# Optimization experiments

Hardware: AMD Instinct MI355X
Metric: run time of the kernel (lower is better)

The kernel has to match this reference:

```python
import jax, jax.numpy as jnp
import numpy as np

N = 100000   # nodes
E = 600000   # edges
G = 512      # graphs in batch
EPS = 1e-5   # LayerNorm eps
IN_DIM = 60 + 2 + 12  # dyn feats*frames + dims + st embedding
H = 128


def setup_inputs() -> dict:
    key = jax.random.key(0)
    ks = jax.random.split(key, 32)
    inp = {
        "x": jax.random.normal(ks[0], (N, 60), jnp.float32),
        "xdims": jax.random.uniform(ks[1], (N, 2), jnp.float32),
        "xsttype": jax.random.randint(ks[2], (N,), 0, 256, jnp.int32),
        "edge_index": jax.random.randint(ks[3], (2, E), 0, N, jnp.int32),
        "batch": jnp.sort(jax.random.randint(ks[4], (N,), 0, G, jnp.int32)),
        "emb": jax.random.normal(ks[5], (256, 12), jnp.float32),
    }
    def lin(k, i, o):
        s = 1.0 / np.sqrt(i)
        return jax.random.uniform(k, (i, o), jnp.float32, -s, s)
    dims = [IN_DIM, H, H]
    for l in range(2):
        i, o = dims[l], dims[l + 1]
        inp[f"Wl{l}"] = lin(ks[6 + 4 * l], i, o)   # lin_l: applied to aggregated neighbors
        inp[f"bl{l}"] = jnp.zeros((o,), jnp.float32)
        inp[f"Wr{l}"] = lin(ks[7 + 4 * l], i, o)   # lin_r: applied to root (no bias, PyG SAGEConv)
        inp[f"g{l}"] = jnp.ones((o,), jnp.float32)   # LayerNorm gamma
        inp[f"bn{l}"] = jnp.zeros((o,), jnp.float32)  # LayerNorm beta
    ld = [2 * H, 50, 50, 10]
    for l in range(3):
        inp[f"Wf{l}"] = lin(ks[20 + l], ld[l], ld[l + 1])
        inp[f"bf{l}"] = jnp.zeros((ld[l + 1],), jnp.float32)
    return inp


def _layer_norm(h, g, b):
    mu = jnp.mean(h, axis=-1, keepdims=True)
    var = jnp.mean(jnp.square(h - mu), axis=-1, keepdims=True)
    return (h - mu) * jax.lax.rsqrt(var + EPS) * g + b


def reference(x, xdims, xsttype, edge_index, batch, emb,
              Wl0, bl0, Wr0, g0, bn0,
              Wl1, bl1, Wr1, g1, bn1,
              Wf0, bf0, Wf1, bf1, Wf2, bf2):
    # node feature assembly: [N, 60+2+12]
    h = jnp.concatenate([x, xdims, emb[xsttype]], axis=1)

    src, dst = edge_index[0], edge_index[1]
    deg = jax.ops.segment_sum(jnp.ones((E,), h.dtype), dst, num_segments=N)
    inv_deg = (1.0 / jnp.maximum(deg, 1.0))[:, None]

    for Wl, bl, Wr, g, bn in ((Wl0, bl0, Wr0, g0, bn0), (Wl1, bl1, Wr1, g1, bn1)):
        # SAGEConv (mean aggr): out = lin_l(mean_j x_j) + lin_r(x_i)
        agg = jax.ops.segment_sum(h[src], dst, num_segments=N) * inv_deg
        h = agg @ Wl + bl + h @ Wr
        h = jax.nn.relu(_layer_norm(h, g, bn))  # dropout inactive (eval)

    # global mean / max pooling over graphs
    cnt = jax.ops.segment_sum(jnp.ones((N,), h.dtype), batch, num_segments=G)
    xmean = jax.ops.segment_sum(h, batch, num_segments=G) / jnp.maximum(cnt, 1.0)[:, None]
    xmax = jax.ops.segment_max(h, batch, num_segments=G)
    z = jnp.concatenate([xmean, xmax], axis=1)  # [G, 2H]

    for Wf, bf in ((Wf0, bf0), (Wf1, bf1), (Wf2, bf2)):
        z = jax.nn.relu(z @ Wf + bf)  # Linear + ReLU + Dropout(eval)
    return z
```

## Files before the change

kernel.cpp:

```cpp
#include <hip/hip_runtime.h>

#define NN 100000
#define NP 100096
#define EE 600000
#define GG 512
#define LN_EPS 1e-5f

typedef __attribute__((ext_vector_type(8))) __bf16 bf16x8;
typedef __attribute__((ext_vector_type(4))) float f32x4;

__device__ __forceinline__ unsigned short f2bf(float f) {
    unsigned int u = __float_as_uint(f);
    u = (u + 0x7fffu + ((u >> 16) & 1u)) >> 16;
    return (unsigned short)u;
}
__device__ __forceinline__ unsigned int pack2(float a, float b) {
    return (unsigned int)f2bf(a) | ((unsigned int)f2bf(b) << 16);
}
__device__ __forceinline__ void acc8(float* s, uint4 v) {
    s[0] += __uint_as_float(v.x << 16);
    s[1] += __uint_as_float(v.x & 0xffff0000u);
    s[2] += __uint_as_float(v.y << 16);
    s[3] += __uint_as_float(v.y & 0xffff0000u);
    s[4] += __uint_as_float(v.z << 16);
    s[5] += __uint_as_float(v.z & 0xffff0000u);
    s[6] += __uint_as_float(v.w << 16);
    s[7] += __uint_as_float(v.w & 0xffff0000u);
}

#define PREP_A (NP * 10)
#define PREP_W0 (128 * 160)
#define PREP_W1 (128 * 256)
#define PREP_TOT (PREP_A + PREP_W0 + PREP_W1 + EE)

__global__ __launch_bounds__(256) void prep_kernel(
    const float* __restrict__ x, const float* __restrict__ xdims,
    const int* __restrict__ stt, const float* __restrict__ emb,
    const int* __restrict__ ei,
    const float* __restrict__ Wl0, const float* __restrict__ Wr0,
    const float* __restrict__ Wl1, const float* __restrict__ Wr1,
    unsigned short* __restrict__ A0,
    unsigned short* __restrict__ Wt0, unsigned short* __restrict__ Wt1,
    int* __restrict__ deg)
{
    int idx = blockIdx.x * 256 + threadIdx.x;
    if (idx < PREP_A) {
        int node = idx / 10;
        int c8 = (idx - node * 10) * 8;
        unsigned short vals[8];
        if (node < NN) {
            int st = stt[node];
            #pragma unroll
            for (int i = 0; i < 8; ++i) {
                int f = c8 + i;
                float v = 0.f;
                if (f < 60)      v = x[node * 60 + f];
                else if (f < 62) v = xdims[node * 2 + (f - 60)];
                else if (f < 74) v = emb[st * 12 + (f - 62)];
                vals[i] = f2bf(v);
            }
        } else {
            #pragma unroll
            for (int i = 0; i < 8; ++i) vals[i] = 0;
        }
        uint4 o;
        o.x = (unsigned)vals[0] | ((unsigned)vals[1] << 16);
        o.y = (unsigned)vals[2] | ((unsigned)vals[3] << 16);
        o.z = (unsigned)vals[4] | ((unsigned)vals[5] << 16);
        o.w = (unsigned)vals[6] | ((unsigned)vals[7] << 16);
        *(uint4*)(A0 + (size_t)node * 160 + 80 + c8) = o;
    } else if (idx < PREP_A + PREP_W0) {
        int j = idx - PREP_A;
        int n = j / 160, k = j - n * 160;
        float v = 0.f;
        if (k < 74)                  v = Wl0[k * 128 + n];
        else if (k >= 80 && k < 154) v = Wr0[(k - 80) * 128 + n];
        Wt0[(size_t)n * 160 + k] = f2bf(v);
    } else if (idx < PREP_A + PREP_W0 + PREP_W1) {
        int j = idx - PREP_A - PREP_W0;
        int n = j >> 8, k = j & 255;
        float v = (k < 128) ? Wl1[k * 128 + n] : Wr1[(k - 128) * 128 + n];
        Wt1[(size_t)n * 256 + k] = f2bf(v);
    } else if (idx < PREP_TOT) {
        int e = idx - PREP_A - PREP_W0 - PREP_W1;
        atomicAdd(&deg[ei[EE + e]], 1);
    }
}

__global__ __launch_bounds__(256) void scan1_kernel(
    const int* __restrict__ deg, int* __restrict__ offs, int* __restrict__ bsum)
{
    __shared__ int ts[256];
    int t = threadIdx.x;
    int base = blockIdx.x * 2048 + t * 8;
    int d[8];
    if (base + 8 <= NN) {
        int4 a = *(const int4*)&deg[base];
        int4 b = *(const int4*)&deg[base + 4];
        d[0]=a.x; d[1]=a.y; d[2]=a.z; d[3]=a.w;
        d[4]=b.x; d[5]=b.y; d[6]=b.z; d[7]=b.w;
    } else {
        #pragma unroll
        for (int i = 0; i < 8; ++i) d[i] = (base + i < NN) ? deg[base + i] : 0;
    }
    int e[8]; int run = 0;
    #pragma unroll
    for (int i = 0; i < 8; ++i) { e[i] = run; run += d[i]; }
    ts[t] = run;
    int tot = run;
    __syncthreads();
    for (int off = 1; off < 256; off <<= 1) {
        int u = (t >= off) ? ts[t - off] : 0;
        __syncthreads();
        ts[t] += u;
        __syncthreads();
    }
    int pre = ts[t] - tot;
    #pragma unroll
    for (int i = 0; i < 8; ++i) if (base + i < NN) offs[base + i] = e[i] + pre;
    if (t == 255) bsum[blockIdx.x] = ts[255];
}

__global__ void scan2_kernel(int* __restrict__ bsum, int nb)
{
    int t = threadIdx.x;
    int v = (t < nb) ? bsum[t] : 0;
    int inc = v;
    for (int off = 1; off < 64; off <<= 1) {
        int u = __shfl_up(inc, off, 64);
        if (t >= off) inc += u;
    }
    if (t < nb) bsum[t] = inc - v;
}

__global__ __launch_bounds__(256) void fill_csr_kernel(
    const int* __restrict__ ei, int* __restrict__ cur,
    const int* __restrict__ offs, const int* __restrict__ bsum,
    int* __restrict__ csr)
{
    int e = blockIdx.x * 256 + threadIdx.x;
    if (e >= EE) return;
    int d = ei[EE + e];
    int p = offs[d] + bsum[d >> 11] + atomicAdd(&cur[d], 1);
    csr[p] = ei[e];
}

__global__ __launch_bounds__(256) void agg0_kernel(
    unsigned short* __restrict__ A0, const int* __restrict__ csr,
    const int* __restrict__ offs, const int* __restrict__ bsum,
    const int* __restrict__ deg)
{
    int node = blockIdx.x * 16 + (threadIdx.x >> 4);
    int lane = threadIdx.x & 15;
    if (node >= NP || lane >= 10) return;
    int d = 0, st = 0;
    if (node < NN) { d = deg[node]; st = offs[node] + bsum[node >> 11]; }
    float iv = 1.0f / (float)(d > 1 ? d : 1);
    float s[8];
    #pragma unroll
    for (int i = 0; i < 8; ++i) s[i] = 0.f;
    int e = 0;
    for (; e + 4 <= d; e += 4) {
        int i0 = csr[st + e],     i1 = csr[st + e + 1];
        int i2 = csr[st + e + 2], i3 = csr[st + e + 3];
        uint4 v0 = *(const uint4*)(A0 + (size_t)i0 * 160 + 80 + lane * 8);
        uint4 v1 = *(const uint4*)(A0 + (size_t)i1 * 160 + 80 + lane * 8);
        uint4 v2 = *(const uint4*)(A0 + (size_t)i2 * 160 + 80 + lane * 8);
        uint4 v3 = *(const uint4*)(A0 + (size_t)i3 * 160 + 80 + lane * 8);
        acc8(s, v0); acc8(s, v1); acc8(s, v2); acc8(s, v3);
    }
    for (; e < d; ++e) {
        int i0 = csr[st + e];
        uint4 v0 = *(const uint4*)(A0 + (size_t)i0 * 160 + 80 + lane * 8);
        acc8(s, v0);
    }
    uint4 o;
    o.x = pack2(s[0] * iv, s[1] * iv);
    o.y = pack2(s[2] * iv, s[3] * iv);
    o.z = pack2(s[4] * iv, s[5] * iv);
    o.w = pack2(s[6] * iv, s[7] * iv);
    *(uint4*)(A0 + (size_t)node * 160 + lane * 8) = o;
}

__global__ __launch_bounds__(256) void agg1_kernel(
    unsigned short* __restrict__ A1, const int* __restrict__ csr,
    const int* __restrict__ offs, const int* __restrict__ bsum,
    const int* __restrict__ deg)
{
    int node = blockIdx.x * 16 + (threadIdx.x >> 4);
    int lane = threadIdx.x & 15;
    if (node >= NP) return;
    int d = 0, st = 0;
    if (node < NN) { d = deg[node]; st = offs[node] + bsum[node >> 11]; }
    float iv = 1.0f / (float)(d > 1 ? d : 1);
    float s[8];
    #pragma unroll
    for (int i = 0; i < 8; ++i) s[i] = 0.f;
    int e = 0;
    for (; e + 4 <= d; e += 4) {
        int i0 = csr[st + e],     i1 = csr[st + e + 1];
        int i2 = csr[st + e + 2], i3 = csr[st + e + 3];
        uint4 v0 = *(const uint4*)(A1 + (size_t)i0 * 256 + 128 + lane * 8);
        uint4 v1 = *(const uint4*)(A1 + (size_t)i1 * 256 + 128 + lane * 8);
        uint4 v2 = *(const uint4*)(A1 + (size_t)i2 * 256 + 128 + lane * 8);
        uint4 v3 = *(const uint4*)(A1 + (size_t)i3 * 256 + 128 + lane * 8);
        acc8(s, v0); acc8(s, v1); acc8(s, v2); acc8(s, v3);
    }
    for (; e < d; ++e) {
        int i0 = csr[st + e];
        uint4 v0 = *(const uint4*)(A1 + (size_t)i0 * 256 + 128 + lane * 8);
        acc8(s, v0);
    }
    uint4 o;
    o.x = pack2(s[0] * iv, s[1] * iv);
    o.y = pack2(s[2] * iv, s[3] * iv);
    o.z = pack2(s[4] * iv, s[5] * iv);
    o.w = pack2(s[6] * iv, s[7] * iv);
    *(uint4*)(A1 + (size_t)node * 256 + 128 - 128 + lane * 8) = o;
}

template<int K, bool POOL>
__global__ __launch_bounds__(256, 4) void gemm_kernel(
    const unsigned short* __restrict__ A,
    const unsigned short* __restrict__ Wt,
    const float* __restrict__ bias, const float* __restrict__ gamma,
    const float* __restrict__ beta,
    unsigned short* __restrict__ outB,
    const int* __restrict__ batch,
    float* __restrict__ psum, int* __restrict__ pmax)
{
    constexpr int KT = K / 32, AS = K + 8, CPR = K / 8;
    constexpr int SMEM = (32 * AS * 2 > 32 * 128 * 4) ? 32 * AS * 2 : 32 * 128 * 4;
    __shared__ __align__(16) char smem[SMEM];
    unsigned short* Asm = (unsigned short*)smem;
    float* Hs = (float*)smem;
    __shared__ __align__(16) float sP[32 * 4];
    __shared__ __align__(16) float qP[32 * 4];
    __shared__ int bS[32];

    const int tid = threadIdx.x;
    const int n0 = blockIdx.x * 32;

    if (POOL && tid < 32) {
        int gn = n0 + tid;
        bS[tid] = (gn < NN) ? batch[gn] : -1;
    }
    for (int i = tid; i < 32 * CPR; i += 256) {
        int node = i / CPR, c = i - node * CPR;
        uint4 v = *(const uint4*)(A + (size_t)(n0 + node) * K + c * 8);
        *(uint4*)(Asm + node * AS + c * 8) = v;
    }

    const int l = tid & 63, w = tid >> 6;
    const int g = l >> 4, c0 = l & 15;
    float bia[2], gam[2], bet[2];
    #pragma unroll
    for (int j = 0; j < 2; ++j) {
        int col = (2 * w + j) * 16 + c0;
        bia[j] = bias[col]; gam[j] = gamma[col]; bet[j] = beta[col];
    }
    const unsigned short* bp0 = Wt + (size_t)((2 * w + 0) * 16 + c0) * K + g * 8;
    const unsigned short* bp1 = Wt + (size_t)((2 * w + 1) * 16 + c0) * K + g * 8;
    const unsigned short* ar0 = Asm + (0 * 16 + c0) * AS + g * 8;
    const unsigned short* ar1 = Asm + (1 * 16 + c0) * AS + g * 8;
    __syncthreads();

    f32x4 acc[2][2];
    acc[0][0] = (f32x4){0.f,0.f,0.f,0.f}; acc[0][1] = (f32x4){0.f,0.f,0.f,0.f};
    acc[1][0] = (f32x4){0.f,0.f,0.f,0.f}; acc[1][1] = (f32x4){0.f,0.f,0.f,0.f};

    #pragma unroll
    for (int kt = 0; kt < KT; ++kt) {
        bf16x8 b0 = *(const bf16x8*)(bp0 + kt * 32);
        bf16x8 b1 = *(const bf16x8*)(bp1 + kt * 32);
        bf16x8 a0 = *(const bf16x8*)(ar0 + kt * 32);
        bf16x8 a1 = *(const bf16x8*)(ar1 + kt * 32);
        acc[0][0] = __builtin_amdgcn_mfma_f32_16x16x32_bf16(a0, b0, acc[0][0], 0, 0, 0);
        acc[0][1] = __builtin_amdgcn_mfma_f32_16x16x32_bf16(a0, b1, acc[0][1], 0, 0, 0);
        acc[1][0] = __builtin_amdgcn_mfma_f32_16x16x32_bf16(a1, b0, acc[1][0], 0, 0, 0);
        acc[1][1] = __builtin_amdgcn_mfma_f32_16x16x32_bf16(a1, b1, acc[1][1], 0, 0, 0);
    }

    #pragma unroll
    for (int m = 0; m < 2; ++m) {
        #pragma unroll
        for (int r = 0; r < 4; ++r) {
            float h0v = acc[m][0][r] + bia[0];
            float h1v = acc[m][1][r] + bia[1];
            float s = h0v + h1v, q = h0v * h0v + h1v * h1v;
            #pragma unroll
            for (int mm = 1; mm < 16; mm <<= 1) {
                s += __shfl_xor(s, mm, 64);
                q += __shfl_xor(q, mm, 64);
            }
            if (c0 == 0) {
                int node = m * 16 + g * 4 + r;
                sP[node * 4 + w] = s;
                qP[node * 4 + w] = q;
            }
        }
    }
    __syncthreads();

    #pragma unroll
    for (int m = 0; m < 2; ++m) {
        #pragma unroll
        for (int r = 0; r < 4; ++r) {
            int node = m * 16 + g * 4 + r;
            float4 sv = *(const float4*)&sP[node * 4];
            float4 qv = *(const float4*)&qP[node * 4];
            float s = (sv.x + sv.y) + (sv.z + sv.w);
            float q = (qv.x + qv.y) + (qv.z + qv.w);
            float mu   = s * (1.f / 128.f);
            float var  = q * (1.f / 128.f) - mu * mu;
            float rinv = rsqrtf(var + LN_EPS);
            float h0v = acc[m][0][r] + bia[0];
            float h1v = acc[m][1][r] + bia[1];
            float v0 = fmaxf(0.f, (h0v - mu) * rinv * gam[0] + bet[0]);
            float v1 = fmaxf(0.f, (h1v - mu) * rinv * gam[1] + bet[1]);
            if (POOL) {
                Hs[node * 128 + (2 * w) * 16 + c0]     = v0;
                Hs[node * 128 + (2 * w + 1) * 16 + c0] = v1;
            } else {
                size_t gn = (size_t)(n0 + node);
                outB[gn * 256 + 128 + (2 * w) * 16 + c0]     = f2bf(v0);
                outB[gn * 256 + 128 + (2 * w + 1) * 16 + c0] = f2bf(v1);
            }
        }
    }
    if (!POOL) return;
    __syncthreads();

    if (tid < 128) {
        int j = tid;
        int curg = -1; float s = 0.f, m = 0.f;
        #pragma unroll 4
        for (int n = 0; n < 32; ++n) {
            int gb = bS[n];
            if (gb < 0) break;
            if (gb != curg) {
                if (curg >= 0) {
                    atomicAdd(&psum[curg * 128 + j], s);
                    atomicMax(&pmax[curg * 128 + j], __float_as_int(m));
                }
                curg = gb; s = 0.f; m = 0.f;
            }
            float v = Hs[n * 128 + j];
            s += v; m = fmaxf(m, v);
        }
        if (curg >= 0) {
            atomicAdd(&psum[curg * 128 + j], s);
            atomicMax(&pmax[curg * 128 + j], __float_as_int(m));
        }
    }
}

__device__ __forceinline__ int lbound(const int* a, int n, int v) {
    int lo = 0, hi = n;
    while (lo < hi) { int mid = (lo + hi) >> 1; if (a[mid] < v) lo = mid + 1; else hi = mid; }
    return lo;
}

__global__ __launch_bounds__(64) void mlp_kernel(
    const float* __restrict__ psum, const int* __restrict__ pmax,
    const int* __restrict__ batch,
    const float* __restrict__ Wf0, const float* __restrict__ bf0,
    const float* __restrict__ Wf1, const float* __restrict__ bf1,
    const float* __restrict__ Wf2, const float* __restrict__ bf2,
    float* __restrict__ out)
{
    __shared__ float z[256];
    __shared__ float t1[50];
    __shared__ float t2[50];
    __shared__ int cS;
    int g = blockIdx.x, t = threadIdx.x;
    if (t == 0) cS = lbound(batch, NN, g + 1) - lbound(batch, NN, g);
    __syncthreads();
    int c = cS;
    float ic = 1.0f / (float)(c > 1 ? c : 1);
    for (int j = t; j < 128; j += 64) {
        z[j]       = psum[g * 128 + j] * ic;
        z[128 + j] = __int_as_float(pmax[g * 128 + j]);
    }
    __syncthreads();
    if (t < 50) {
        float a = bf0[t];
        for (int k = 0; k < 256; ++k) a = fmaf(z[k], Wf0[k * 50 + t], a);
        t1[t] = fmaxf(a, 0.0f);
    }
    __syncthreads();
    if (t < 50) {
        float a = bf1[t];
        for (int k = 0; k < 50; ++k) a = fmaf(t1[k], Wf1[k * 50 + t], a);
        t2[t] = fmaxf(a, 0.0f);
    }
    __syncthreads();
    if (t < 10) {
        float a = bf2[t];
        for (int k = 0; k < 50; ++k) a = fmaf(t2[k], Wf2[k * 10 + t], a);
        out[g * 10 + t] = fmaxf(a, 0.0f);
    }
}

extern "C" void kernel_launch(void* const* d_in, const int* in_sizes, int n_in,
                              void* d_out, int out_size, void* d_ws, size_t ws_size,
                              hipStream_t stream)
{
    const float* x     = (const float*)d_in[0];
    const float* xdims = (const float*)d_in[1];
    const int*   stt   = (const int*)d_in[2];
    const int*   ei    = (const int*)d_in[3];
    const int*   batch = (const int*)d_in[4];
    const float* emb   = (const float*)d_in[5];
    const float* Wl0   = (const float*)d_in[6];
    const float* bl0   = (const float*)d_in[7];
    const float* Wr0   = (const float*)d_in[8];
    const float* g0    = (const float*)d_in[9];
    const float* bn0   = (const float*)d_in[10];
    const float* Wl1   = (const float*)d_in[11];
    const float* bl1   = (const float*)d_in[12];
    const float* Wr1   = (const float*)d_in[13];
    const float* g1    = (const float*)d_in[14];
    const float* bn1   = (const float*)d_in[15];
    const float* Wf0   = (const float*)d_in[16];
    const float* bf0   = (const float*)d_in[17];
    const float* Wf1   = (const float*)d_in[18];
    const float* bf1   = (const float*)d_in[19];
    const float* Wf2   = (const float*)d_in[20];
    const float* bf2   = (const float*)d_in[21];

    char* w = (char*)d_ws;
    unsigned short* A0  = (unsigned short*)w; w += (size_t)NP * 160 * 2;
    unsigned short* A1  = (unsigned short*)w; w += (size_t)NP * 256 * 2;
    unsigned short* Wt0 = (unsigned short*)w; w += (size_t)128 * 160 * 2;
    unsigned short* Wt1 = (unsigned short*)w; w += (size_t)128 * 256 * 2;
    int*   csr    = (int*)w;   w += (size_t)EE * 4;
    int*   offs   = (int*)w;   w += (size_t)NN * 4;
    int*   bsum   = (int*)w;   w += 1024;
    char* zbeg = w;
    int*   deg  = (int*)w;   w += (size_t)NP * 4;
    int*   cur  = (int*)w;   w += (size_t)NN * 4;
    float* psum = (float*)w; w += (size_t)GG * 128 * 4;
    int*   pmax = (int*)w;   w += (size_t)GG * 128 * 4;
    size_t zsz = (size_t)(w - zbeg);

    hipMemsetAsync(zbeg, 0, zsz, stream);

    prep_kernel<<<(PREP_TOT + 255) / 256, 256, 0, stream>>>(
        x, xdims, stt, emb, ei, Wl0, Wr0, Wl1, Wr1, A0, Wt0, Wt1, deg);

    int nb = (NN + 2047) / 2048;
    scan1_kernel<<<nb, 256, 0, stream>>>(deg, offs, bsum);
    scan2_kernel<<<1, 64, 0, stream>>>(bsum, nb);
    fill_csr_kernel<<<(EE + 255) / 256, 256, 0, stream>>>(ei, cur, offs, bsum, csr);

    agg0_kernel<<<NP / 16, 256, 0, stream>>>(A0, csr, offs, bsum, deg);
    gemm_kernel<160, false><<<NP / 32, 256, 0, stream>>>(
        A0, Wt0, bl0, g0, bn0, A1, nullptr, nullptr, nullptr);
    agg1_kernel<<<NP / 16, 256, 0, stream>>>(A1, csr, offs, bsum, deg);
    gemm_kernel<256, true><<<NP / 32, 256, 0, stream>>>(
        A1, Wt1, bl1, g1, bn1, nullptr, batch, psum, pmax);

    mlp_kernel<<<GG, 64, 0, stream>>>(psum, pmax, batch, Wf0, bf0, Wf1, bf1, Wf2, bf2,
                                      (float*)d_out);
}
```

Baseline: 310.9 us.

## Split root and aggregate buffers into compact arrays; persistent GEMM with register-resident weights

The interleaved [agg|root] row buffers are replaced by separate compact arrays, so each gather in the aggregation kernels reads from a denser, smaller buffer and gets better cache-line use. The GEMM kernels become persistent: a fixed grid of 1024 blocks loops over the 32-node tiles and keeps the weight fragments in registers for the whole launch instead of reloading them for every tile. The cost is higher register pressure (KT*2 bf16x8 fragments per thread, up to 16 for K=256), which may lower occupancy. There are also extra __syncthreads per tile iteration.

```diff
diff --git a/kernel.cpp b/kernel.cpp
--- a/kernel.cpp
+++ b/kernel.cpp
@@ -2,6 +2,8 @@
 
 #define NN 100000
 #define NP 100096
+#define NT (NP / 32)
+#define GB 1024
 #define EE 600000
 #define GG 512
 #define LN_EPS 1e-5f
@@ -39,7 +41,7 @@
     const int* __restrict__ ei,
     const float* __restrict__ Wl0, const float* __restrict__ Wr0,
     const float* __restrict__ Wl1, const float* __restrict__ Wr1,
-    unsigned short* __restrict__ A0,
+    unsigned short* __restrict__ H0r,
     unsigned short* __restrict__ Wt0, unsigned short* __restrict__ Wt1,
     int* __restrict__ deg)
 {
@@ -68,7 +70,7 @@
         o.y = (unsigned)vals[2] | ((unsigned)vals[3] << 16);
         o.z = (unsigned)vals[4] | ((unsigned)vals[5] << 16);
         o.w = (unsigned)vals[6] | ((unsigned)vals[7] << 16);
-        *(uint4*)(A0 + (size_t)node * 160 + 80 + c8) = o;
+        *(uint4*)(H0r + (size_t)node * 80 + c8) = o;
     } else if (idx < PREP_A + PREP_W0) {
         int j = idx - PREP_A;
         int n = j / 160, k = j - n * 160;
@@ -146,9 +148,9 @@
 }
 
 __global__ __launch_bounds__(256) void agg0_kernel(
-    unsigned short* __restrict__ A0, const int* __restrict__ csr,
-    const int* __restrict__ offs, const int* __restrict__ bsum,
-    const int* __restrict__ deg)
+    const unsigned short* __restrict__ H0r, unsigned short* __restrict__ A0g,
+    const int* __restrict__ csr, const int* __restrict__ offs,
+    const int* __restrict__ bsum, const int* __restrict__ deg)
 {
     int node = blockIdx.x * 16 + (threadIdx.x >> 4);
     int lane = threadIdx.x & 15;
@@ -163,15 +165,15 @@
     for (; e + 4 <= d; e += 4) {
         int i0 = csr[st + e],     i1 = csr[st + e + 1];
         int i2 = csr[st + e + 2], i3 = csr[st + e + 3];
-        uint4 v0 = *(const uint4*)(A0 + (size_t)i0 * 160 + 80 + lane * 8);
-        uint4 v1 = *(const uint4*)(A0 + (size_t)i1 * 160 + 80 + lane * 8);
-        uint4 v2 = *(const uint4*)(A0 + (size_t)i2 * 160 + 80 + lane * 8);
-        uint4 v3 = *(const uint4*)(A0 + (size_t)i3 * 160 + 80 + lane * 8);
+        uint4 v0 = *(const uint4*)(H0r + (size_t)i0 * 80 + lane * 8);
+        uint4 v1 = *(const uint4*)(H0r + (size_t)i1 * 80 + lane * 8);
+        uint4 v2 = *(const uint4*)(H0r + (size_t)i2 * 80 + lane * 8);
+        uint4 v3 = *(const uint4*)(H0r + (size_t)i3 * 80 + lane * 8);
         acc8(s, v0); acc8(s, v1); acc8(s, v2); acc8(s, v3);
     }
     for (; e < d; ++e) {
         int i0 = csr[st + e];
-        uint4 v0 = *(const uint4*)(A0 + (size_t)i0 * 160 + 80 + lane * 8);
+        uint4 v0 = *(const uint4*)(H0r + (size_t)i0 * 80 + lane * 8);
         acc8(s, v0);
     }
     uint4 o;
@@ -179,13 +181,13 @@
     o.y = pack2(s[2] * iv, s[3] * iv);
     o.z = pack2(s[4] * iv, s[5] * iv);
     o.w = pack2(s[6] * iv, s[7] * iv);
-    *(uint4*)(A0 + (size_t)node * 160 + lane * 8) = o;
+    *(uint4*)(A0g + (size_t)node * 80 + lane * 8) = o;
 }
 
 __global__ __launch_bounds__(256) void agg1_kernel(
-    unsigned short* __restrict__ A1, const int* __restrict__ csr,
-    const int* __restrict__ offs, const int* __restrict__ bsum,
-    const int* __restrict__ deg)
+    const unsigned short* __restrict__ H1, unsigned short* __restrict__ A1g,
+    const int* __restrict__ csr, const int* __restrict__ offs,
+    const int* __restrict__ bsum, const int* __restrict__ deg)
 {
     int node = blockIdx.x * 16 + (threadIdx.x >> 4);
     int lane = threadIdx.x & 15;
@@ -200,15 +202,15 @@
     for (; e + 4 <= d; e += 4) {
         int i0 = csr[st + e],     i1 = csr[st + e + 1];
         int i2 = csr[st + e + 2], i3 = csr[st + e + 3];
-        uint4 v0 = *(const uint4*)(A1 + (size_t)i0 * 256 + 128 + lane * 8);
-        uint4 v1 = *(const uint4*)(A1 + (size_t)i1 * 256 + 128 + lane * 8);
-        uint4 v2 = *(const uint4*)(A1 + (size_t)i2 * 256 + 128 + lane * 8);
-        uint4 v3 = *(const uint4*)(A1 + (size_t)i3 * 256 + 128 + lane * 8);
+        uint4 v0 = *(const uint4*)(H1 + (size_t)i0 * 128 + lane * 8);
+        uint4 v1 = *(const uint4*)(H1 + (size_t)i1 * 128 + lane * 8);
+        uint4 v2 = *(const uint4*)(H1 + (size_t)i2 * 128 + lane * 8);
+        uint4 v3 = *(const uint4*)(H1 + (size_t)i3 * 128 + lane * 8);
         acc8(s, v0); acc8(s, v1); acc8(s, v2); acc8(s, v3);
     }
     for (; e < d; ++e) {
         int i0 = csr[st + e];
-        uint4 v0 = *(const uint4*)(A1 + (size_t)i0 * 256 + 128 + lane * 8);
+        uint4 v0 = *(const uint4*)(H1 + (size_t)i0 * 128 + lane * 8);
         acc8(s, v0);
     }
     uint4 o;
@@ -216,20 +218,21 @@
     o.y = pack2(s[2] * iv, s[3] * iv);
     o.z = pack2(s[4] * iv, s[5] * iv);
     o.w = pack2(s[6] * iv, s[7] * iv);
-    *(uint4*)(A1 + (size_t)node * 256 + 128 - 128 + lane * 8) = o;
+    *(uint4*)(A1g + (size_t)node * 128 + lane * 8) = o;
 }
 
 template<int K, bool POOL>
 __global__ __launch_bounds__(256, 4) void gemm_kernel(
-    const unsigned short* __restrict__ A,
+    const unsigned short* __restrict__ Ag,
+    const unsigned short* __restrict__ Hr,
     const unsigned short* __restrict__ Wt,
     const float* __restrict__ bias, const float* __restrict__ gamma,
     const float* __restrict__ beta,
-    unsigned short* __restrict__ outB,
+    unsigned short* __restrict__ outH,
     const int* __restrict__ batch,
     float* __restrict__ psum, int* __restrict__ pmax)
 {
-    constexpr int KT = K / 32, AS = K + 8, CPR = K / 8;
+    constexpr int KT = K / 32, AS = K + 8, CPR = K / 8, CPRh = CPR / 2, RH = K / 2;
     constexpr int SMEM = (32 * AS * 2 > 32 * 128 * 4) ? 32 * AS * 2 : 32 * 128 * 4;
     __shared__ __align__(16) char smem[SMEM];
     unsigned short* Asm = (unsigned short*)smem;
@@ -239,118 +242,129 @@
     __shared__ int bS[32];
 
     const int tid = threadIdx.x;
-    const int n0 = blockIdx.x * 32;
-
-    if (POOL && tid < 32) {
-        int gn = n0 + tid;
-        bS[tid] = (gn < NN) ? batch[gn] : -1;
-    }
-    for (int i = tid; i < 32 * CPR; i += 256) {
-        int node = i / CPR, c = i - node * CPR;
-        uint4 v = *(const uint4*)(A + (size_t)(n0 + node) * K + c * 8);
-        *(uint4*)(Asm + node * AS + c * 8) = v;
-    }
-
     const int l = tid & 63, w = tid >> 6;
     const int g = l >> 4, c0 = l & 15;
+
+    bf16x8 bfr[KT][2];
+    #pragma unroll
+    for (int j = 0; j < 2; ++j) {
+        const unsigned short* bp = Wt + (size_t)((2 * w + j) * 16 + c0) * K + g * 8;
+        #pragma unroll
+        for (int kt = 0; kt < KT; ++kt)
+            bfr[kt][j] = *(const bf16x8*)(bp + kt * 32);
+    }
     float bia[2], gam[2], bet[2];
     #pragma unroll
     for (int j = 0; j < 2; ++j) {
         int col = (2 * w + j) * 16 + c0;
         bia[j] = bias[col]; gam[j] = gamma[col]; bet[j] = beta[col];
     }
-    const unsigned short* bp0 = Wt + (size_t)((2 * w + 0) * 16 + c0) * K + g * 8;
-    const unsigned short* bp1 = Wt + (size_t)((2 * w + 1) * 16 + c0) * K + g * 8;
     const unsigned short* ar0 = Asm + (0 * 16 + c0) * AS + g * 8;
     const unsigned short* ar1 = Asm + (1 * 16 + c0) * AS + g * 8;
-    __syncthreads();
-
-    f32x4 acc[2][2];
-    acc[0][0] = (f32x4){0.f,0.f,0.f,0.f}; acc[0][1] = (f32x4){0.f,0.f,0.f,0.f};
-    acc[1][0] = (f32x4){0.f,0.f,0.f,0.f}; acc[1][1] = (f32x4){0.f,0.f,0.f,0.f};
-
-    #pragma unroll
-    for (int kt = 0; kt < KT; ++kt) {
-        bf16x8 b0 = *(const bf16x8*)(bp0 + kt * 32);
-        bf16x8 b1 = *(const bf16x8*)(bp1 + kt * 32);
-        bf16x8 a0 = *(const bf16x8*)(ar0 + kt * 32);
-        bf16x8 a1 = *(const bf16x8*)(ar1 + kt * 32);
-        acc[0][0] = __builtin_amdgcn_mfma_f32_16x16x32_bf16(a0, b0, acc[0][0], 0, 0, 0);
-        acc[0][1] = __builtin_amdgcn_mfma_f32_16x16x32_bf16(a0, b1, acc[0][1], 0, 0, 0);
-        acc[1][0] = __builtin_amdgcn_mfma_f32_16x16x32_bf16(a1, b0, acc[1][0], 0, 0, 0);
-        acc[1][1] = __builtin_amdgcn_mfma_f32_16x16x32_bf16(a1, b1, acc[1][1], 0, 0, 0);
-    }
-
-    #pragma unroll
-    for (int m = 0; m < 2; ++m) {
+
+    for (int t = blockIdx.x; t < NT; t += gridDim.x) {
+        const int n0 = t * 32;
+        if (POOL && tid < 32) {
+            int gn = n0 + tid;
+            bS[tid] = (gn < NN) ? batch[gn] : -1;
+        }
+        for (int i = tid; i < 32 * CPR; i += 256) {
+            int node = i / CPR, c = i - node * CPR;
+            size_t gn = (size_t)(n0 + node);
+            const unsigned short* src = (c < CPRh)
+                ? (Ag + gn * RH + c * 8)
+                : (Hr + gn * RH + (c - CPRh) * 8);
+            uint4 v = *(const uint4*)src;
+            *(uint4*)(Asm + node * AS + c * 8) = v;
+        }
+        __syncthreads();
+
+        f32x4 acc[2][2];
+        acc[0][0] = (f32x4){0.f,0.f,0.f,0.f}; acc[0][1] = (f32x4){0.f,0.f,0.f,0.f};
+        acc[1][0] = (f32x4){0.f,0.f,0.f,0.f}; acc[1][1] = (f32x4){0.f,0.f,0.f,0.f};
         #pragma unroll
-        for (int r = 0; r < 4; ++r) {
-            float h0v = acc[m][0][r] + bia[0];
-            float h1v = acc[m][1][r] + bia[1];
-            float s = h0v + h1v, q = h0v * h0v + h1v * h1v;
+        for (int kt = 0; kt < KT; ++kt) {
+            bf16x8 a0 = *(const bf16x8*)(ar0 + kt * 32);
+            bf16x8 a1 = *(const bf16x8*)(ar1 + kt * 32);
+            acc[0][0] = __builtin_amdgcn_mfma_f32_16x16x32_bf16(a0, bfr[kt][0], acc[0][0], 0, 0, 0);
+            acc[0][1] = __builtin_amdgcn_mfma_f32_16x16x32_bf16(a0, bfr[kt][1], acc[0][1], 0, 0, 0);
+            acc[1][0] = __builtin_amdgcn_mfma_f32_16x16x32_bf16(a1, bfr[kt][0], acc[1][0], 0, 0, 0);
+            acc[1][1] = __builtin_amdgcn_mfma_f32_16x16x32_bf16(a1, bfr[kt][1], acc[1][1], 0, 0, 0);
+        }
+
+        #pragma unroll
+        for (int m = 0; m < 2; ++m) {
             #pragma unroll
-            for (int mm = 1; mm < 16; mm <<= 1) {
-                s += __shfl_xor(s, mm, 64);
-                q += __shfl_xor(q, mm, 64);
+            for (int r = 0; r < 4; ++r) {
+                float h0v = acc[m][0][r] + bia[0];
+                float h1v = acc[m][1][r] + bia[1];
+                float s = h0v + h1v, q = h0v * h0v + h1v * h1v;
+                #pragma unroll
+                for (int mm = 1; mm < 16; mm <<= 1) {
+                    s += __shfl_xor(s, mm, 64);
+                    q += __shfl_xor(q, mm, 64);
+                }
+                if (c0 == 0) {
+                    int node = m * 16 + g * 4 + r;
+                    sP[node * 4 + w] = s;
+                    qP[node * 4 + w] = q;
+                }
             }
-            if (c0 == 0) {
+        }
+        __syncthreads();
+
+        #pragma unroll
+        for (int m = 0; m < 2; ++m) {
+            #pragma unroll
+            for (int r = 0; r < 4; ++r) {
                 int node = m * 16 + g * 4 + r;
-                sP[node * 4 + w] = s;
-                qP[node * 4 + w] = q;
+                float4 sv = *(const float4*)&sP[node * 4];
+                float4 qv = *(const float4*)&qP[node * 4];
+                float s = (sv.x + sv.y) + (sv.z + sv.w);
+                float q = (qv.x + qv.y) + (qv.z + qv.w);
+                float mu   = s * (1.f / 128.f);
+                float var  = q * (1.f / 128.f) - mu * mu;
+                float rinv = rsqrtf(var + LN_EPS);
+                float h0v = acc[m][0][r] + bia[0];
+                float h1v = acc[m][1][r] + bia[1];
+                float v0 = fmaxf(0.f, (h0v - mu) * rinv * gam[0] + bet[0]);
+                float v1 = fmaxf(0.f, (h1v - mu) * rinv * gam[1] + bet[1]);
+                if (POOL) {
+                    Hs[node * 128 + (2 * w) * 16 + c0]     = v0;
+                    Hs[node * 128 + (2 * w + 1) * 16 + c0] = v1;
+                } else {
+                    size_t gn = (size_t)(n0 + node);
+                    outH[gn * 128 + (2 * w) * 16 + c0]     = f2bf(v0);
+                    outH[gn * 128 + (2 * w + 1) * 16 + c0] = f2bf(v1);
+                }
             }
         }
-    }
-    __syncthreads();
-
-    #pragma unroll
-    for (int m = 0; m < 2; ++m) {
-        #pragma unroll
-        for (int r = 0; r < 4; ++r) {
-            int node = m * 16 + g * 4 + r;
-            float4 sv = *(const float4*)&sP[node * 4];
-            float4 qv = *(const float4*)&qP[node * 4];
-            float s = (sv.x + sv.y) + (sv.z + sv.w);
-            float q = (qv.x + qv.y) + (qv.z + qv.w);
-            float mu   = s * (1.f / 128.f);
-            float var  = q * (1.f / 128.f) - mu * mu;
-            float rinv = rsqrtf(var + LN_EPS);
-            float h0v = acc[m][0][r] + bia[0];
-            float h1v = acc[m][1][r] + bia[1];
-            float v0 = fmaxf(0.f, (h0v - mu) * rinv * gam[0] + bet[0]);
-            float v1 = fmaxf(0.f, (h1v - mu) * rinv * gam[1] + bet[1]);
-            if (POOL) {
-                Hs[node * 128 + (2 * w) * 16 + c0]     = v0;
-                Hs[node * 128 + (2 * w + 1) * 16 + c0] = v1;
-            } else {
-                size_t gn = (size_t)(n0 + node);
-                outB[gn * 256 + 128 + (2 * w) * 16 + c0]     = f2bf(v0);
-                outB[gn * 256 + 128 + (2 * w + 1) * 16 + c0] = f2bf(v1);
-            }
-        }
-    }
-    if (!POOL) return;
-    __syncthreads();
-
-    if (tid < 128) {
-        int j = tid;
-        int curg = -1; float s = 0.f, m = 0.f;
-        #pragma unroll 4
-        for (int n = 0; n < 32; ++n) {
-            int gb = bS[n];
-            if (gb < 0) break;
-            if (gb != curg) {
+        __syncthreads();
+
+        if (POOL) {
+            if (tid < 128) {
+                int j = tid;
+                int curg = -1; float s = 0.f, m = 0.f;
+                #pragma unroll 4
+                for (int n = 0; n < 32; ++n) {
+                    int gb = bS[n];
+                    if (gb < 0) break;
+                    if (gb != curg) {
+                        if (curg >= 0) {
+                            atomicAdd(&psum[curg * 128 + j], s);
+                            atomicMax(&pmax[curg * 128 + j], __float_as_int(m));
+                        }
+                        curg = gb; s = 0.f; m = 0.f;
+                    }
+                    float v = Hs[n * 128 + j];
+                    s += v; m = fmaxf(m, v);
+                }
                 if (curg >= 0) {
                     atomicAdd(&psum[curg * 128 + j], s);
                     atomicMax(&pmax[curg * 128 + j], __float_as_int(m));
                 }
-                curg = gb; s = 0.f; m = 0.f;
             }
-            float v = Hs[n * 128 + j];
-            s += v; m = fmaxf(m, v);
-        }
-        if (curg >= 0) {
-            atomicAdd(&psum[curg * 128 + j], s);
-            atomicMax(&pmax[curg * 128 + j], __float_as_int(m));
+            __syncthreads();
         }
     }
 }
@@ -430,8 +444,10 @@
     const float* bf2   = (const float*)d_in[21];
 
     char* w = (char*)d_ws;
-    unsigned short* A0  = (unsigned short*)w; w += (size_t)NP * 160 * 2;
-    unsigned short* A1  = (unsigned short*)w; w += (size_t)NP * 256 * 2;
+    unsigned short* H0r = (unsigned short*)w; w += (size_t)NP * 80 * 2;
+    unsigned short* A0g = (unsigned short*)w; w += (size_t)NP * 80 * 2;
+    unsigned short* H1  = (unsigned short*)w; w += (size_t)NP * 128 * 2;
+    unsigned short* A1g = (unsigned short*)w; w += (size_t)NP * 128 * 2;
     unsigned short* Wt0 = (unsigned short*)w; w += (size_t)128 * 160 * 2;
     unsigned short* Wt1 = (unsigned short*)w; w += (size_t)128 * 256 * 2;
     int*   csr    = (int*)w;   w += (size_t)EE * 4;
@@ -447,19 +463,19 @@
     hipMemsetAsync(zbeg, 0, zsz, stream);
 
     prep_kernel<<<(PREP_TOT + 255) / 256, 256, 0, stream>>>(
-        x, xdims, stt, emb, ei, Wl0, Wr0, Wl1, Wr1, A0, Wt0, Wt1, deg);
+        x, xdims, stt, emb, ei, Wl0, Wr0, Wl1, Wr1, H0r, Wt0, Wt1, deg);
 
     int nb = (NN + 2047) / 2048;
     scan1_kernel<<<nb, 256, 0, stream>>>(deg, offs, bsum);
     scan2_kernel<<<1, 64, 0, stream>>>(bsum, nb);
     fill_csr_kernel<<<(EE + 255) / 256, 256, 0, stream>>>(ei, cur, offs, bsum, csr);
 
-    agg0_kernel<<<NP / 16, 256, 0, stream>>>(A0, csr, offs, bsum, deg);
-    gemm_kernel<160, false><<<NP / 32, 256, 0, stream>>>(
-        A0, Wt0, bl0, g0, bn0, A1, nullptr, nullptr, nullptr);
-    agg1_kernel<<<NP / 16, 256, 0, stream>>>(A1, csr, offs, bsum, deg);
-    gemm_kernel<256, true><<<NP / 32, 256, 0, stream>>>(
-        A1, Wt1, bl1, g1, bn1, nullptr, batch, psum, pmax);
+    agg0_kernel<<<NP / 16, 256, 0, stream>>>(H0r, A0g, csr, offs, bsum, deg);
+    gemm_kernel<160, false><<<GB, 256, 0, stream>>>(
+        A0g, H0r, Wt0, bl0, g0, bn0, H1, nullptr, nullptr, nullptr);
+    agg1_kernel<<<NP / 16, 256, 0, stream>>>(H1, A1g, csr, offs, bsum, deg);
+    gemm_kernel<256, true><<<GB, 256, 0, stream>>>(
+        A1g, H1, Wt1, bl1, g1, bn1, nullptr, batch, psum, pmax);
 
     mlp_kernel<<<GG, 64, 0, stream>>>(psum, pmax, batch, Wf0, bf0, Wf1, bf1, Wf2, bf2,
                                       (float*)d_out);
```

New measurement: 329.9 us. +6.1%, slower.
